# Optimization experiments

Hardware: AMD Instinct MI355X
Metric: run time of the kernel (lower is better)

Reference implementation:

```python
import jax, jax.numpy as jnp
import numpy as np

D = 4096

def setup_inputs() -> dict:
    key = jax.random.key(0)
    ks = jax.random.split(key, 14)
    s = 1.0 / np.sqrt(D)
    return {
        "x": jax.random.normal(ks[0], (D,), jnp.float32),
        "state_xx": jax.random.normal(ks[1], (D,), jnp.float32),
        "aa": jax.random.normal(ks[2], (D,), jnp.float32),
        "bb": jax.random.uniform(ks[3], (D,), jnp.float32) + 0.5,  # positive running denom
        "pp": jax.random.normal(ks[4], (D,), jnp.float32),
        "w_key": jax.random.normal(ks[5], (D, D), jnp.float32) * s,
        "w_val": jax.random.normal(ks[6], (D, D), jnp.float32) * s,
        "w_rec": jax.random.normal(ks[7], (D, D), jnp.float32) * s,
        "w_out": jax.random.normal(ks[8], (D, D), jnp.float32) * s,
        "t_decay": -jax.random.uniform(ks[9], (D,), jnp.float32),  # module stores -exp(time_decay) < 0
        "t_first": jax.random.normal(ks[10], (D,), jnp.float32) * 0.5,
        "t_mix_k": jax.random.uniform(ks[11], (D,), jnp.float32),
        "t_mix_v": jax.random.uniform(ks[12], (D,), jnp.float32),
        "t_mix_r": jax.random.uniform(ks[13], (D,), jnp.float32),
    }


def reference(x, state_xx, aa, bb, pp, w_key, w_val, w_rec, w_out,
              t_decay, t_first, t_mix_k, t_mix_v, t_mix_r):
    # token mixing with previous token (state_xx)
    xk = x * t_mix_k + state_xx * (1.0 - t_mix_k)
    xv = x * t_mix_v + state_xx * (1.0 - t_mix_v)
    xr = x * t_mix_r + state_xx * (1.0 - t_mix_r)

    r = jax.nn.sigmoid(w_rec @ xr)
    k = w_key @ xk
    v = w_val @ xv

    # stabilized WKV output using current token bonus t_first
    ww = t_first + k
    p = jnp.maximum(pp, ww)
    e1 = jnp.exp(pp - p)
    e2 = jnp.exp(ww - p)
    a = e1 * aa + e2 * v
    b = e1 * bb + e2

    # stabilized state update with decay
    ww2 = pp + t_decay
    p2 = jnp.maximum(ww2, k)
    e1b = jnp.exp(ww2 - p2)
    e2b = jnp.exp(k - p2)
    new_aa = e1b * aa + e2b * v
    new_bb = e1b * bb + e2b
    new_pp = p2

    y = w_out @ (r * (a / b))
    # (output, new state_xx, new aa, new bb, new pp)
    return (y, x, new_aa, new_bb, new_pp)
```

## Files before the change

kernel.cpp:

```cpp
#include <hip/hip_runtime.h>

#define DIM 4096
#define BLK 256
#define ROWS 4

__device__ __forceinline__ float dot4(float4 a, float4 b) {
  return a.x * b.x + a.y * b.y + a.z * b.z + a.w * b.w;
}

__device__ __forceinline__ float4 mix4(float4 xi, float4 si, float4 m) {
  float4 r;
  r.x = fmaf(xi.x - si.x, m.x, si.x);
  r.y = fmaf(xi.y - si.y, m.y, si.y);
  r.z = fmaf(xi.z - si.z, m.z, si.z);
  r.w = fmaf(xi.w - si.w, m.w, si.w);
  return r;
}

__global__ void __launch_bounds__(BLK) fused3_kernel(
    const float* __restrict__ x, const float* __restrict__ sxx,
    const float* __restrict__ tmk, const float* __restrict__ tmv,
    const float* __restrict__ tmr,
    const float* __restrict__ wr, const float* __restrict__ wk,
    const float* __restrict__ wv,
    const float* __restrict__ aa, const float* __restrict__ bb,
    const float* __restrict__ pp,
    const float* __restrict__ t_decay, const float* __restrict__ t_first,
    float* __restrict__ rab, float* __restrict__ out_x,
    float* __restrict__ out_aa, float* __restrict__ out_bb,
    float* __restrict__ out_pp) {
  const int t = threadIdx.x;
  const int row0 = blockIdx.x * ROWS;

  const float4* x4 = (const float4*)x;
  const float4* s4 = (const float4*)sxx;
  const float4* mk4 = (const float4*)tmk;
  const float4* mv4 = (const float4*)tmv;
  const float4* mr4 = (const float4*)tmr;

  float4 fxr[4], fxk[4], fxv[4];
#pragma unroll
  for (int j = 0; j < 4; ++j) {
    int idx = t + j * BLK;
    float4 xi = x4[idx], si = s4[idx];
    fxk[j] = mix4(xi, si, mk4[idx]);
    fxv[j] = mix4(xi, si, mv4[idx]);
    fxr[j] = mix4(xi, si, mr4[idx]);
  }

  float accr[ROWS], acck[ROWS], accv[ROWS];
#pragma unroll
  for (int r = 0; r < ROWS; ++r) { accr[r] = acck[r] = accv[r] = 0.f; }

#pragma unroll
  for (int r = 0; r < ROWS; ++r) {
    const float4* wrp = (const float4*)(wr + (size_t)(row0 + r) * DIM);
    const float4* wkp = (const float4*)(wk + (size_t)(row0 + r) * DIM);
    const float4* wvp = (const float4*)(wv + (size_t)(row0 + r) * DIM);
#pragma unroll
    for (int j = 0; j < 4; ++j) {
      int idx = t + j * BLK;
      accr[r] += dot4(wrp[idx], fxr[j]);
      acck[r] += dot4(wkp[idx], fxk[j]);
      accv[r] += dot4(wvp[idx], fxv[j]);
    }
  }

#pragma unroll
  for (int off = 32; off > 0; off >>= 1) {
#pragma unroll
    for (int r = 0; r < ROWS; ++r) {
      accr[r] += __shfl_down(accr[r], off);
      acck[r] += __shfl_down(acck[r], off);
      accv[r] += __shfl_down(accv[r], off);
    }
  }
  __shared__ float red[4][ROWS * 3];
  const int wave = t >> 6, lane = t & 63;
  if (lane == 0) {
#pragma unroll
    for (int r = 0; r < ROWS; ++r) {
      red[wave][r * 3 + 0] = accr[r];
      red[wave][r * 3 + 1] = acck[r];
      red[wave][r * 3 + 2] = accv[r];
    }
  }
  __syncthreads();

  if (t < ROWS) {
    const int row = row0 + t;
    float sr = red[0][t * 3 + 0] + red[1][t * 3 + 0] + red[2][t * 3 + 0] + red[3][t * 3 + 0];
    float sk = red[0][t * 3 + 1] + red[1][t * 3 + 1] + red[2][t * 3 + 1] + red[3][t * 3 + 1];
    float sv = red[0][t * 3 + 2] + red[1][t * 3 + 2] + red[2][t * 3 + 2] + red[3][t * 3 + 2];

    float rsig = 1.0f / (1.0f + expf(-sr));
    float ppi = pp[row], aai = aa[row], bbi = bb[row];
    float ww = t_first[row] + sk;
    float p = fmaxf(ppi, ww);
    float e1 = expf(ppi - p), e2 = expf(ww - p);
    float a = e1 * aai + e2 * sv;
    float b = e1 * bbi + e2;
    rab[row] = rsig * (a / b);
    float ww2 = ppi + t_decay[row];
    float p2 = fmaxf(ww2, sk);
    float e1b = expf(ww2 - p2), e2b = expf(sk - p2);
    out_x[row]  = x[row];
    out_aa[row] = e1b * aai + e2b * sv;
    out_bb[row] = e1b * bbi + e2b;
    out_pp[row] = p2;
  }
}

__global__ void __launch_bounds__(BLK) matvec_out_kernel(
    const float* __restrict__ w, const float* __restrict__ xin,
    float* __restrict__ y) {
  const int t = threadIdx.x;
  const int row0 = blockIdx.x * ROWS;
  const float4* x4 = (const float4*)xin;

  float4 fx[4];
#pragma unroll
  for (int j = 0; j < 4; ++j) fx[j] = x4[t + j * BLK];

  float acc[ROWS];
#pragma unroll
  for (int r = 0; r < ROWS; ++r) acc[r] = 0.f;

#pragma unroll
  for (int r = 0; r < ROWS; ++r) {
    const float4* wp = (const float4*)(w + (size_t)(row0 + r) * DIM);
#pragma unroll
    for (int j = 0; j < 4; ++j) acc[r] += dot4(wp[t + j * BLK], fx[j]);
  }

#pragma unroll
  for (int off = 32; off > 0; off >>= 1) {
#pragma unroll
    for (int r = 0; r < ROWS; ++r) acc[r] += __shfl_down(acc[r], off);
  }
  __shared__ float red[4][ROWS];
  const int wave = t >> 6, lane = t & 63;
  if (lane == 0) {
#pragma unroll
    for (int r = 0; r < ROWS; ++r) red[wave][r] = acc[r];
  }
  __syncthreads();
  if (t < ROWS) {
    y[row0 + t] = red[0][t] + red[1][t] + red[2][t] + red[3][t];
  }
}

extern "C" void kernel_launch(void* const* d_in, const int* in_sizes, int n_in,
                              void* d_out, int out_size, void* d_ws, size_t ws_size,
                              hipStream_t stream) {
  const float* x       = (const float*)d_in[0];
  const float* sxx     = (const float*)d_in[1];
  const float* aa      = (const float*)d_in[2];
  const float* bb      = (const float*)d_in[3];
  const float* pp      = (const float*)d_in[4];
  const float* w_key   = (const float*)d_in[5];
  const float* w_val   = (const float*)d_in[6];
  const float* w_rec   = (const float*)d_in[7];
  const float* w_out   = (const float*)d_in[8];
  const float* t_decay = (const float*)d_in[9];
  const float* t_first = (const float*)d_in[10];
  const float* t_mix_k = (const float*)d_in[11];
  const float* t_mix_v = (const float*)d_in[12];
  const float* t_mix_r = (const float*)d_in[13];

  float* out    = (float*)d_out;
  float* y      = out;
  float* out_x  = out + DIM;
  float* out_aa = out + 2 * DIM;
  float* out_bb = out + 3 * DIM;
  float* out_pp = out + 4 * DIM;

  float* rab = (float*)d_ws;

  fused3_kernel<<<DIM / ROWS, BLK, 0, stream>>>(
      x, sxx, t_mix_k, t_mix_v, t_mix_r, w_rec, w_key, w_val,
      aa, bb, pp, t_decay, t_first,
      rab, out_x, out_aa, out_bb, out_pp);
  matvec_out_kernel<<<DIM / ROWS, BLK, 0, stream>>>(w_out, rab, y);
}
```

Before: 262.1 us.

## Assign one wavefront per matrix row and stage mixed vectors in LDS

```diff
diff --git a/kernel.cpp b/kernel.cpp
--- a/kernel.cpp
+++ b/kernel.cpp
@@ -1,8 +1,9 @@
 #include <hip/hip_runtime.h>
 
 #define DIM 4096
-#define BLK 256
 #define ROWS 4
+#define BLK1 768
+#define BLK2 256
 
 __device__ __forceinline__ float dot4(float4 a, float4 b) {
   return a.x * b.x + a.y * b.y + a.z * b.z + a.w * b.w;
@@ -17,7 +18,7 @@
   return r;
 }
 
-__global__ void __launch_bounds__(BLK) fused3_kernel(
+__global__ void __launch_bounds__(BLK1, 6) fused3_kernel(
     const float* __restrict__ x, const float* __restrict__ sxx,
     const float* __restrict__ tmk, const float* __restrict__ tmv,
     const float* __restrict__ tmr,
@@ -29,125 +30,92 @@
     float* __restrict__ rab, float* __restrict__ out_x,
     float* __restrict__ out_aa, float* __restrict__ out_bb,
     float* __restrict__ out_pp) {
+  __shared__ float4 xmix[3][DIM / 4];
+  __shared__ float red[3 * ROWS];
+
   const int t = threadIdx.x;
-  const int row0 = blockIdx.x * ROWS;
 
-  const float4* x4 = (const float4*)x;
-  const float4* s4 = (const float4*)sxx;
+  const float4* x4  = (const float4*)x;
+  const float4* s4  = (const float4*)sxx;
   const float4* mk4 = (const float4*)tmk;
   const float4* mv4 = (const float4*)tmv;
   const float4* mr4 = (const float4*)tmr;
 
-  float4 fxr[4], fxk[4], fxv[4];
+  for (int idx = t; idx < DIM / 4; idx += BLK1) {
+    float4 xi = x4[idx], si = s4[idx];
+    xmix[0][idx] = mix4(xi, si, mr4[idx]);
+    xmix[1][idx] = mix4(xi, si, mk4[idx]);
+    xmix[2][idx] = mix4(xi, si, mv4[idx]);
+  }
+  __syncthreads();
+
+  const int wave = t >> 6, lane = t & 63;
+  const int mat = wave >> 2;
+  const int r   = wave & 3;
+  const int row = blockIdx.x * ROWS + r;
+
+  const float* wbase = (mat == 0) ? wr : ((mat == 1) ? wk : wv);
+  const float4* wp = (const float4*)(wbase + (size_t)row * DIM);
+  const float4* xp = xmix[mat];
+
+  float acc = 0.f;
 #pragma unroll
-  for (int j = 0; j < 4; ++j) {
-    int idx = t + j * BLK;
-    float4 xi = x4[idx], si = s4[idx];
-    fxk[j] = mix4(xi, si, mk4[idx]);
-    fxv[j] = mix4(xi, si, mv4[idx]);
-    fxr[j] = mix4(xi, si, mr4[idx]);
-  }
-
-  float accr[ROWS], acck[ROWS], accv[ROWS];
-#pragma unroll
-  for (int r = 0; r < ROWS; ++r) { accr[r] = acck[r] = accv[r] = 0.f; }
-
-#pragma unroll
-  for (int r = 0; r < ROWS; ++r) {
-    const float4* wrp = (const float4*)(wr + (size_t)(row0 + r) * DIM);
-    const float4* wkp = (const float4*)(wk + (size_t)(row0 + r) * DIM);
-    const float4* wvp = (const float4*)(wv + (size_t)(row0 + r) * DIM);
-#pragma unroll
-    for (int j = 0; j < 4; ++j) {
-      int idx = t + j * BLK;
-      accr[r] += dot4(wrp[idx], fxr[j]);
-      acck[r] += dot4(wkp[idx], fxk[j]);
-      accv[r] += dot4(wvp[idx], fxv[j]);
-    }
+  for (int i = 0; i < 16; ++i) {
+    acc += dot4(wp[i * 64 + lane], xp[i * 64 + lane]);
   }
 
 #pragma unroll
-  for (int off = 32; off > 0; off >>= 1) {
-#pragma unroll
-    for (int r = 0; r < ROWS; ++r) {
-      accr[r] += __shfl_down(accr[r], off);
-      acck[r] += __shfl_down(acck[r], off);
-      accv[r] += __shfl_down(accv[r], off);
-    }
-  }
-  __shared__ float red[4][ROWS * 3];
-  const int wave = t >> 6, lane = t & 63;
-  if (lane == 0) {
-#pragma unroll
-    for (int r = 0; r < ROWS; ++r) {
-      red[wave][r * 3 + 0] = accr[r];
-      red[wave][r * 3 + 1] = acck[r];
-      red[wave][r * 3 + 2] = accv[r];
-    }
-  }
+  for (int off = 32; off > 0; off >>= 1) acc += __shfl_down(acc, off);
+  if (lane == 0) red[mat * ROWS + r] = acc;
   __syncthreads();
 
   if (t < ROWS) {
-    const int row = row0 + t;
-    float sr = red[0][t * 3 + 0] + red[1][t * 3 + 0] + red[2][t * 3 + 0] + red[3][t * 3 + 0];
-    float sk = red[0][t * 3 + 1] + red[1][t * 3 + 1] + red[2][t * 3 + 1] + red[3][t * 3 + 1];
-    float sv = red[0][t * 3 + 2] + red[1][t * 3 + 2] + red[2][t * 3 + 2] + red[3][t * 3 + 2];
+    const int orow = blockIdx.x * ROWS + t;
+    float sr = red[0 * ROWS + t];
+    float sk = red[1 * ROWS + t];
+    float sv = red[2 * ROWS + t];
 
     float rsig = 1.0f / (1.0f + expf(-sr));
-    float ppi = pp[row], aai = aa[row], bbi = bb[row];
-    float ww = t_first[row] + sk;
-    float p = fmaxf(ppi, ww);
+    float ppi = pp[orow], aai = aa[orow], bbi = bb[orow];
+    float ww = t_first[orow] + sk;
+    float p  = fmaxf(ppi, ww);
     float e1 = expf(ppi - p), e2 = expf(ww - p);
     float a = e1 * aai + e2 * sv;
     float b = e1 * bbi + e2;
-    rab[row] = rsig * (a / b);
-    float ww2 = ppi + t_decay[row];
-    float p2 = fmaxf(ww2, sk);
+    rab[orow] = rsig * (a / b);
+    float ww2 = ppi + t_decay[orow];
+    float p2  = fmaxf(ww2, sk);
     float e1b = expf(ww2 - p2), e2b = expf(sk - p2);
-    out_x[row]  = x[row];
-    out_aa[row] = e1b * aai + e2b * sv;
-    out_bb[row] = e1b * bbi + e2b;
-    out_pp[row] = p2;
+    out_x[orow]  = x[orow];
+    out_aa[orow] = e1b * aai + e2b * sv;
+    out_bb[orow] = e1b * bbi + e2b;
+    out_pp[orow] = p2;
   }
 }
 
-__global__ void __launch_bounds__(BLK) matvec_out_kernel(
+__global__ void __launch_bounds__(BLK2) matvec_out_kernel(
     const float* __restrict__ w, const float* __restrict__ xin,
     float* __restrict__ y) {
+  __shared__ float4 xs[DIM / 4];
   const int t = threadIdx.x;
-  const int row0 = blockIdx.x * ROWS;
   const float4* x4 = (const float4*)xin;
+#pragma unroll
+  for (int k = 0; k < 4; ++k) xs[t + k * BLK2] = x4[t + k * BLK2];
+  __syncthreads();
 
-  float4 fx[4];
+  const int wave = t >> 6, lane = t & 63;
+  const int row = blockIdx.x * 4 + wave;
+  const float4* wp = (const float4*)(w + (size_t)row * DIM);
+
+  float acc = 0.f;
 #pragma unroll
-  for (int j = 0; j < 4; ++j) fx[j] = x4[t + j * BLK];
-
-  float acc[ROWS];
-#pragma unroll
-  for (int r = 0; r < ROWS; ++r) acc[r] = 0.f;
-
-#pragma unroll
-  for (int r = 0; r < ROWS; ++r) {
-    const float4* wp = (const float4*)(w + (size_t)(row0 + r) * DIM);
-#pragma unroll
-    for (int j = 0; j < 4; ++j) acc[r] += dot4(wp[t + j * BLK], fx[j]);
+  for (int i = 0; i < 16; ++i) {
+    acc += dot4(wp[i * 64 + lane], xs[i * 64 + lane]);
   }
 
 #pragma unroll
-  for (int off = 32; off > 0; off >>= 1) {
-#pragma unroll
-    for (int r = 0; r < ROWS; ++r) acc[r] += __shfl_down(acc[r], off);
-  }
-  __shared__ float red[4][ROWS];
-  const int wave = t >> 6, lane = t & 63;
-  if (lane == 0) {
-#pragma unroll
-    for (int r = 0; r < ROWS; ++r) red[wave][r] = acc[r];
-  }
-  __syncthreads();
-  if (t < ROWS) {
-    y[row0 + t] = red[0][t] + red[1][t] + red[2][t] + red[3][t];
-  }
+  for (int off = 32; off > 0; off >>= 1) acc += __shfl_down(acc, off);
+  if (lane == 0) y[row] = acc;
 }
 
 extern "C" void kernel_launch(void* const* d_in, const int* in_sizes, int n_in,
@@ -177,9 +145,9 @@
 
   float* rab = (float*)d_ws;
 
-  fused3_kernel<<<DIM / ROWS, BLK, 0, stream>>>(
+  fused3_kernel<<<DIM / ROWS, BLK1, 0, stream>>>(
       x, sxx, t_mix_k, t_mix_v, t_mix_r, w_rec, w_key, w_val,
       aa, bb, pp, t_decay, t_first,
       rab, out_x, out_aa, out_bb, out_pp);
-  matvec_out_kernel<<<DIM / ROWS, BLK, 0, stream>>>(w_out, rab, y);
+  matvec_out_kernel<<<DIM / 4, BLK2, 0, stream>>>(w_out, rab, y);
 }
```

New measurement: 262.7 us. Within noise of the previous version (+0.2%).
